# Kernel optimization log

Hardware: AMD Instinct MI355X
Metric: run time of the kernel (lower is better)

## Reference

```python
import jax, jax.numpy as jnp
import numpy as np

B, S = 4, 2048
D_MODEL, N_HEADS, D_KV = 1024, 16, 64
NUM_BUCKETS, MAX_DIST = 32, 128


def _relative_position_bucket(relative_position, num_buckets=NUM_BUCKETS, max_distance=MAX_DIST):
    # bidirectional (encoder) variant, faithful to FlaxT5Attention._relative_position_bucket
    num_buckets = num_buckets // 2
    relative_buckets = (relative_position > 0).astype(jnp.int32) * num_buckets
    rp = jnp.abs(relative_position)
    max_exact = num_buckets // 2
    is_small = rp < max_exact
    rp_large = max_exact + (
        jnp.log(rp.astype(jnp.float32) / max_exact)
        / np.log(max_distance / max_exact)
        * (num_buckets - max_exact)
    )
    rp_large = jnp.minimum(rp_large, num_buckets - 1)
    return relative_buckets + jnp.where(is_small, rp, rp_large.astype(jnp.int32))


def setup_inputs() -> dict:
    key = jax.random.key(0)
    ks = jax.random.split(key, 6)
    return {
        "hidden_states": jax.random.normal(ks[0], (B, S, D_MODEL), jnp.float32),
        "mask": jnp.zeros((B, S), jnp.float32),  # additive mask, 0 = attend
        "wq": jax.random.normal(ks[1], (D_MODEL, N_HEADS * D_KV), jnp.float32) * 0.02,
        "wk": jax.random.normal(ks[2], (D_MODEL, N_HEADS * D_KV), jnp.float32) * 0.02,
        "wv": jax.random.normal(ks[3], (D_MODEL, N_HEADS * D_KV), jnp.float32) * 0.02,
        "wo": jax.random.normal(ks[4], (N_HEADS * D_KV, D_MODEL), jnp.float32) * 0.02,
        "rel_bias": jax.random.normal(ks[5], (NUM_BUCKETS, N_HEADS), jnp.float32) * 0.02,
    }


def reference(hidden_states, mask, wq, wk, wv, wo, rel_bias):
    b, s, _ = hidden_states.shape
    # QKV projections, split heads -> [B, S, H, D]
    q = (hidden_states @ wq).reshape(b, s, N_HEADS, D_KV)
    k = (hidden_states @ wk).reshape(b, s, N_HEADS, D_KV)
    v = (hidden_states @ wv).reshape(b, s, N_HEADS, D_KV)

    # relative position bias -> [1, H, S, S]
    pos = jnp.arange(s, dtype=jnp.int32)
    relative_position = pos[None, :] - pos[:, None]  # memory - query
    buckets = _relative_position_bucket(relative_position)
    position_bias = rel_bias[buckets].transpose(2, 0, 1)[None]  # [1,H,S,S]
    # encoder path: additive mask expanded to [B,1,1,K]
    position_bias = position_bias + mask[:, None, None, :]

    # flax dot_product_attention_weights scales q by 1/sqrt(depth)
    scores = jnp.einsum("bqhd,bkhd->bhqk", q / jnp.sqrt(jnp.float32(D_KV)), k)
    attn_weights = jax.nn.softmax(scores + position_bias, axis=-1)

    attn_output = jnp.einsum("bhqk,bkhd->bqhd", attn_weights, v)
    attn_output = attn_output.reshape(b, s, N_HEADS * D_KV) @ wo
    return attn_output, position_bias
```

## Files before the change

kernel.cpp:

```cpp
#include <hip/hip_runtime.h>
#include <hip/hip_bf16.h>

typedef __attribute__((ext_vector_type(8))) short bf16x8;
typedef __attribute__((ext_vector_type(8))) unsigned short u16x8;
typedef __attribute__((ext_vector_type(4))) float f32x4;

#define B_   4
#define S_   2048
#define H_   16
#define DKV  64
#define DM   1024

static __device__ __forceinline__ f32x4 mfma16(bf16x8 a, bf16x8 b, f32x4 c){
  return __builtin_amdgcn_mfma_f32_16x16x32_bf16(a, b, c, 0, 0, 0);
}
static __device__ __forceinline__ unsigned short f2b(float f){
  union { __hip_bfloat16 b; unsigned short u; } x;
  x.b = __float2bfloat16(f);
  return x.u;
}

__global__ void cast_h_kernel(const float* __restrict__ in, unsigned short* __restrict__ out, int n4){
  int i = blockIdx.x * 256 + threadIdx.x;
  if (i >= n4) return;
  float4 v = reinterpret_cast<const float4*>(in)[i];
  ushort4 r;
  r.x = f2b(v.x); r.y = f2b(v.y); r.z = f2b(v.z); r.w = f2b(v.w);
  reinterpret_cast<ushort4*>(out)[i] = r;
}

__global__ void transpose_w_kernel(const float* __restrict__ w0, const float* __restrict__ w1,
                                   const float* __restrict__ w2, const float* __restrict__ w3,
                                   unsigned short* o0, unsigned short* o1,
                                   unsigned short* o2, unsigned short* o3){
  int z = blockIdx.z;
  const float* src = (z==0) ? w0 : (z==1) ? w1 : (z==2) ? w2 : w3;
  unsigned short* dst = (z==0) ? o0 : (z==1) ? o1 : (z==2) ? o2 : o3;
  __shared__ float tile[32][33];
  int bx = blockIdx.x * 32, by = blockIdx.y * 32;
  int tx = threadIdx.x, ty = threadIdx.y;
  #pragma unroll
  for (int i = 0; i < 32; i += 8)
    tile[ty + i][tx] = src[(size_t)(by + ty + i) * DM + bx + tx];
  __syncthreads();
  #pragma unroll
  for (int i = 0; i < 32; i += 8)
    dst[(size_t)(bx + ty + i) * DM + by + tx] = f2b(tile[tx][ty + i]);
}

__global__ void build_table_kernel(const float* __restrict__ rel_bias, float* __restrict__ table_t){
  int i = blockIdx.x * 256 + threadIdx.x;
  if (i >= 16 * 4095) return;
  int h = i / 4095;
  int idx = i - h * 4095;
  int rel = idx - 2047;
  int bucket = (rel > 0) ? 16 : 0;
  int rp = (rel < 0) ? -rel : rel;
  int off;
  if (rp < 8) off = rp;
  else off = 8 + (rp>=12) + (rp>=16) + (rp>=23) + (rp>=32) + (rp>=46) + (rp>=64) + (rp>=91);
  table_t[i] = rel_bias[(bucket + off) * 16 + h];
}

__global__ void posbias_kernel(const float* __restrict__ relb, const float* __restrict__ mask,
                               float* __restrict__ out){
  __shared__ float rbh[32];
  int row = blockIdx.x;
  int q = row & (S_ - 1);
  int h = (row >> 11) & (H_ - 1);
  int b = row >> 15;
  int tid = threadIdx.x;
  if (tid < 32) rbh[tid] = relb[tid * 16 + h];
  __syncthreads();
  const float* mrow = mask + b * S_;
  float* orow = out + (size_t)row * S_;
  int k0 = tid * 8;
  #pragma unroll
  for (int c = 0; c < 2; ++c){
    float4 mv = *(const float4*)(mrow + k0 + c * 4);
    float4 v;
    #pragma unroll
    for (int j = 0; j < 4; ++j){
      int k = k0 + c * 4 + j;
      int rel = k - q;
      int bucket = (rel > 0) ? 16 : 0;
      int rp = (rel < 0) ? -rel : rel;
      int off = (rp < 8) ? rp
              : 8 + (rp>=12) + (rp>=16) + (rp>=23) + (rp>=32) + (rp>=46) + (rp>=64) + (rp>=91);
      (&v.x)[j] = rbh[bucket + off] + (&mv.x)[j];
    }
    *(float4*)(orow + k0 + c*4) = v;
  }
}

template<int MODE>
__global__ __launch_bounds__(256, 2) void gemm_bt_kernel(
    const unsigned short* __restrict__ A, const unsigned short* __restrict__ Bt,
    void* __restrict__ outp, int M, int N, int K, float scale)
{
  __shared__ __align__(16) unsigned short As[128 * 40];
  __shared__ __align__(16) unsigned short Bs[128 * 40];
  int tid = threadIdx.x; int lane = tid & 63; int w = tid >> 6;
  int wr = w >> 1, wc = w & 1;
  int n0 = blockIdx.x * 128, m0 = blockIdx.y * 128;
  const char* Ab = (const char*)A;
  const char* Bb = (const char*)Bt;
  size_t Kb = (size_t)K * 2;

  int srow = (tid * 16) >> 6;
  int scolb = (tid * 16) & 63;

  f32x4 acc[4][4];
  #pragma unroll
  for (int i = 0; i < 4; ++i)
    #pragma unroll
    for (int j = 0; j < 4; ++j) acc[i][j] = (f32x4){0.f, 0.f, 0.f, 0.f};

  bf16x8 ar[2], br[2];
  auto gload = [&](int kt){
    size_t k0b = (size_t)kt * 64;
    #pragma unroll
    for (int c = 0; c < 2; ++c){
      int row = srow + c * 64;
      ar[c] = *(const bf16x8*)(Ab + (size_t)(m0 + row) * Kb + k0b + scolb);
      br[c] = *(const bf16x8*)(Bb + (size_t)(n0 + row) * Kb + k0b + scolb);
    }
  };
  auto lwrite = [&](){
    #pragma unroll
    for (int c = 0; c < 2; ++c){
      int row = srow + c * 64;
      *(bf16x8*)((char*)As + row * 80 + scolb) = ar[c];
      *(bf16x8*)((char*)Bs + row * 80 + scolb) = br[c];
    }
  };

  int nk = K >> 5;
  gload(0);
  lwrite();
  for (int kt = 0; kt < nk; ++kt){
    __syncthreads();
    if (kt + 1 < nk) gload(kt + 1);
    bf16x8 af[4], bfr[4];
    #pragma unroll
    for (int f = 0; f < 4; ++f){
      int row = wr * 64 + f * 16 + (lane & 15);
      af[f] = *(const bf16x8*)((const char*)As + row * 80 + (lane >> 4) * 16);
    }
    #pragma unroll
    for (int f = 0; f < 4; ++f){
      int row = wc * 64 + f * 16 + (lane & 15);
      bfr[f] = *(const bf16x8*)((const char*)Bs + row * 80 + (lane >> 4) * 16);
    }
    #pragma unroll
    for (int i = 0; i < 4; ++i)
      #pragma unroll
      for (int j = 0; j < 4; ++j)
        acc[i][j] = mfma16(af[i], bfr[j], acc[i][j]);
    __syncthreads();
    if (kt + 1 < nk) lwrite();
  }

  #pragma unroll
  for (int i = 0; i < 4; ++i){
    #pragma unroll
    for (int j = 0; j < 4; ++j){
      #pragma unroll
      for (int r = 0; r < 4; ++r){
        int m = m0 + wr * 64 + i * 16 + ((lane >> 4) * 4) + r;
        int n = n0 + wc * 64 + j * 16 + (lane & 15);
        if (MODE == 0){
          ((float*)outp)[(size_t)m * N + n] = acc[i][j][r] * scale;
        } else {
          int sel = n >> 10, nn = n & 1023;
          float v = acc[i][j][r] * (sel == 0 ? 0.125f : 1.0f);
          int b = m >> 11, s = m & 2047, hh = nn >> 6, d = nn & 63;
          ((unsigned short*)outp)[(size_t)sel * 8388608 +
              (((size_t)(b * H_ + hh) * S_) + s) * DKV + d] = f2b(v);
        }
      }
    }
  }
}

__global__ __launch_bounds__(256, 2) void attn_mfma_kernel(
    const unsigned short* __restrict__ Qp, const unsigned short* __restrict__ Kp,
    const unsigned short* __restrict__ Vp, const float* __restrict__ table_t,
    const float* __restrict__ mask, unsigned short* __restrict__ outp)
{
  __shared__ __align__(16) unsigned short Ks[64][72];
  __shared__ __align__(16) unsigned short Vs[64][72];
  __shared__ __align__(16) unsigned short Ps[4][16][72];
  __shared__ float bias_s[127];
  __shared__ float mask_s[64];

  int bid = blockIdx.x;
  int qt = bid & 31; int h = (bid >> 5) & 15; int b = bid >> 9;
  int qb = qt * 64;
  const unsigned short* qptr = Qp + ((size_t)(b * H_ + h) * S_ + qb) * DKV;
  const unsigned short* kptr = Kp + (size_t)(b * H_ + h) * S_ * DKV;
  const unsigned short* vptr = Vp + (size_t)(b * H_ + h) * S_ * DKV;
  int tid = threadIdx.x; int lane = tid & 63; int w = tid >> 6;

  bf16x8 qf[2];
  {
    const unsigned short* qrow = qptr + (size_t)(w * 16 + (lane & 15)) * DKV + 8 * (lane >> 4);
    qf[0] = *(const bf16x8*)qrow;
    qf[1] = *(const bf16x8*)(qrow + 32);
  }
  float m_r[4], l_r[4];
  f32x4 o_acc[4];
  #pragma unroll
  for (int r = 0; r < 4; ++r){ m_r[r] = -1e30f; l_r[r] = 0.f; }
  #pragma unroll
  for (int d = 0; d < 4; ++d) o_acc[d] = (f32x4){0.f, 0.f, 0.f, 0.f};

  int bias_base = h * 4095 + (2047 - qb - 63);

  int skey = tid & 63;
  int sd0  = (tid >> 6) * 16;

  u16x8 ka, kb2, va, vb2;
  float biasr = 0.f, maskr = 0.f;
  auto gload = [&](int k0){
    const unsigned short* krow = kptr + (size_t)(k0 + skey) * DKV + sd0;
    const unsigned short* vrow = vptr + (size_t)(k0 + skey) * DKV + sd0;
    ka  = *(const u16x8*)krow;
    kb2 = *(const u16x8*)(krow + 8);
    va  = *(const u16x8*)vrow;
    vb2 = *(const u16x8*)(vrow + 8);
    if (tid < 127) biasr = table_t[bias_base + k0 + tid];
    else if (tid >= 128 && tid < 192) maskr = mask[b * S_ + k0 + (tid - 128)];
  };
  auto lwrite = [&](){
    *(u16x8*)&Ks[skey][sd0]     = ka;
    *(u16x8*)&Ks[skey][sd0 + 8] = kb2;
    #pragma unroll
    for (int j = 0; j < 8; ++j){
      Vs[sd0 + j][skey]     = va[j];
      Vs[sd0 + 8 + j][skey] = vb2[j];
    }
    if (tid < 127) bias_s[tid] = biasr;
    else if (tid < 192) mask_s[tid - 128] = maskr;
  };

  gload(0);
  lwrite();
  for (int k0 = 0; k0 < S_; k0 += 64){
    __syncthreads();
    if (k0 + 64 < S_) gload(k0 + 64);

    f32x4 sc[4];
    #pragma unroll
    for (int kb = 0; kb < 4; ++kb){
      sc[kb] = (f32x4){0.f, 0.f, 0.f, 0.f};
      #pragma unroll
      for (int ks = 0; ks < 2; ++ks){
        int row = kb * 16 + (lane & 15);
        bf16x8 kf = *(const bf16x8*)&Ks[row][ks * 32 + (lane >> 4) * 8];
        sc[kb] = mfma16(qf[ks], kf, sc[kb]);
      }
    }
    float t[4][4];
    float tmax[4] = {-1e30f, -1e30f, -1e30f, -1e30f};
    #pragma unroll
    for (int kb = 0; kb < 4; ++kb){
      int k_l = kb * 16 + (lane & 15);
      float mk = mask_s[k_l];
      #pragma unroll
      for (int r = 0; r < 4; ++r){
        int q_l = w * 16 + (lane >> 4) * 4 + r;
        float tv = sc[kb][r] + bias_s[k_l - q_l + 63] + mk;
        t[kb][r] = tv;
        tmax[r] = fmaxf(tmax[r], tv);
      }
    }
    #pragma unroll
    for (int r = 0; r < 4; ++r){
      #pragma unroll
      for (int off = 1; off < 16; off <<= 1)
        tmax[r] = fmaxf(tmax[r], __shfl_xor(tmax[r], off, 64));
    }
    float scl[4];
    #pragma unroll
    for (int r = 0; r < 4; ++r){
      float mn = fmaxf(m_r[r], tmax[r]);
      scl[r] = __expf(m_r[r] - mn);
      m_r[r] = mn;
    }
    float rs[4] = {0.f, 0.f, 0.f, 0.f};
    #pragma unroll
    for (int kb = 0; kb < 4; ++kb)
      #pragma unroll
      for (int r = 0; r < 4; ++r){
        float p = __expf(t[kb][r] - m_r[r]);
        t[kb][r] = p;
        rs[r] += p;
      }
    #pragma unroll
    for (int r = 0; r < 4; ++r){
      #pragma unroll
      for (int off = 1; off < 16; off <<= 1)
        rs[r] += __shfl_xor(rs[r], off, 64);
      l_r[r] = l_r[r] * scl[r] + rs[r];
      o_acc[0][r] *= scl[r]; o_acc[1][r] *= scl[r];
      o_acc[2][r] *= scl[r]; o_acc[3][r] *= scl[r];
    }
    #pragma unroll
    for (int kb = 0; kb < 4; ++kb)
      #pragma unroll
      for (int r = 0; r < 4; ++r){
        int prow = (lane >> 4) * 4 + r;
        int pcol = kb * 16 + (lane & 15);
        Ps[w][prow][pcol] = f2b(t[kb][r]);
      }
    bf16x8 pa[2];
    #pragma unroll
    for (int ks = 0; ks < 2; ++ks)
      pa[ks] = *(const bf16x8*)&Ps[w][lane & 15][ks * 32 + (lane >> 4) * 8];
    #pragma unroll
    for (int db = 0; db < 4; ++db)
      #pragma unroll
      for (int ks = 0; ks < 2; ++ks){
        bf16x8 vf = *(const bf16x8*)&Vs[db * 16 + (lane & 15)][ks * 32 + (lane >> 4) * 8];
        o_acc[db] = mfma16(pa[ks], vf, o_acc[db]);
      }

    __syncthreads();
    if (k0 + 64 < S_) lwrite();
  }

  #pragma unroll
  for (int r = 0; r < 4; ++r){
    float inv = 1.0f / l_r[r];
    int qg = qb + w * 16 + (lane >> 4) * 4 + r;
    size_t rowoff = ((size_t)b * S_ + qg) * DM + h * DKV;
    #pragma unroll
    for (int db = 0; db < 4; ++db)
      outp[rowoff + db * 16 + (lane & 15)] = f2b(o_acc[db][r] * inv);
  }
}

extern "C" void kernel_launch(void* const* d_in, const int* in_sizes, int n_in,
                              void* d_out, int out_size, void* d_ws, size_t ws_size,
                              hipStream_t stream) {
  const float* hs   = (const float*)d_in[0];
  const float* msk  = (const float*)d_in[1];
  const float* wq   = (const float*)d_in[2];
  const float* wk   = (const float*)d_in[3];
  const float* wv   = (const float*)d_in[4];
  const float* wo   = (const float*)d_in[5];
  const float* relb = (const float*)d_in[6];

  float* out_attn = (float*)d_out;
  float* out_pb   = (float*)d_out + (size_t)B_ * S_ * DM;
  char* ws = (char*)out_pb;

  unsigned short* h_bf  = (unsigned short*)(ws + 0);
  unsigned short* wqkv_t= (unsigned short*)(ws + 16777216);
  unsigned short* wk_t  = (unsigned short*)(ws + 18874368);
  unsigned short* wv_t  = (unsigned short*)(ws + 20971520);
  unsigned short* wo_t  = (unsigned short*)(ws + 23068672);
  unsigned short* qkv_b = (unsigned short*)(ws + 25165824);
  unsigned short* k_b   = (unsigned short*)(ws + 41943040);
  unsigned short* v_b   = (unsigned short*)(ws + 58720256);
  float*          tabl  = (float*)(ws + 75497472);

  cast_h_kernel<<<8192, 256, 0, stream>>>(hs, h_bf, (B_ * S_ * DM) / 4);
  transpose_w_kernel<<<dim3(32, 32, 4), dim3(32, 8), 0, stream>>>(wq, wk, wv, wo,
                                                                  wqkv_t, wk_t, wv_t, wo_t);
  build_table_kernel<<<256, 256, 0, stream>>>(relb, tabl);

  gemm_bt_kernel<1><<<dim3(24, 64), 256, 0, stream>>>(h_bf, wqkv_t, qkv_b, 8192, 3072, 1024, 1.0f);

  attn_mfma_kernel<<<B_ * H_ * 32, 256, 0, stream>>>(qkv_b, k_b, v_b, tabl, msk, h_bf);

  gemm_bt_kernel<0><<<dim3(8, 64), 256, 0, stream>>>(h_bf, wo_t, out_attn, 8192, 1024, 1024, 1.0f);

  posbias_kernel<<<B_ * H_ * S_, 256, 0, stream>>>(relb, msk, out_pb);
}
```

Before: 541.7 us.

## Fuse position-bias output writes into attention kernel when workspace available

The attention kernel now also writes the [B,H,S,S] position-bias output from the bias and mask values it already holds in shared memory, which removes the separate posbias kernel. Intermediates move to the provided workspace so the position-bias region of the output is no longer used as scratch. This overlaps the large output store with attention compute, but adds global store traffic and work inside the attention loop. The fused path is taken only if the workspace is large enough; otherwise the old sequence runs.

```diff
diff --git a/kernel.cpp b/kernel.cpp
--- a/kernel.cpp
+++ b/kernel.cpp
@@ -183,10 +183,12 @@
   }
 }
 
+template<int FUSE_PB>
 __global__ __launch_bounds__(256, 2) void attn_mfma_kernel(
     const unsigned short* __restrict__ Qp, const unsigned short* __restrict__ Kp,
     const unsigned short* __restrict__ Vp, const float* __restrict__ table_t,
-    const float* __restrict__ mask, unsigned short* __restrict__ outp)
+    const float* __restrict__ mask, unsigned short* __restrict__ outp,
+    float* __restrict__ pb_out)
 {
   __shared__ __align__(16) unsigned short Ks[64][72];
   __shared__ __align__(16) unsigned short Vs[64][72];
@@ -219,6 +221,9 @@
 
   int skey = tid & 63;
   int sd0  = (tid >> 6) * 16;
+  int pq = tid >> 2;
+  int pk = (tid & 3) * 16;
+  float* pb_row = FUSE_PB ? (pb_out + ((size_t)((b * H_ + h) * S_) + qb + pq) * S_ + pk) : nullptr;
 
   u16x8 ka, kb2, va, vb2;
   float biasr = 0.f, maskr = 0.f;
@@ -261,6 +266,20 @@
         sc[kb] = mfma16(qf[ks], kf, sc[kb]);
       }
     }
+
+    if (FUSE_PB){
+      #pragma unroll
+      for (int c = 0; c < 4; ++c){
+        float4 v;
+        #pragma unroll
+        for (int j = 0; j < 4; ++j){
+          int kl = pk + c * 4 + j;
+          (&v.x)[j] = bias_s[kl - pq + 63] + mask_s[kl];
+        }
+        *(float4*)(pb_row + k0 + c * 4) = v;
+      }
+    }
+
     float t[4][4];
     float tmax[4] = {-1e30f, -1e30f, -1e30f, -1e30f};
     #pragma unroll
@@ -354,7 +373,10 @@
 
   float* out_attn = (float*)d_out;
   float* out_pb   = (float*)d_out + (size_t)B_ * S_ * DM;
-  char* ws = (char*)out_pb;
+
+  const size_t SCRATCH_NEED = 76021760;
+  bool fuse = (ws_size >= SCRATCH_NEED) && (d_ws != nullptr);
+  char* ws = fuse ? (char*)d_ws : (char*)out_pb;
 
   unsigned short* h_bf  = (unsigned short*)(ws + 0);
   unsigned short* wqkv_t= (unsigned short*)(ws + 16777216);
@@ -373,9 +395,12 @@
 
   gemm_bt_kernel<1><<<dim3(24, 64), 256, 0, stream>>>(h_bf, wqkv_t, qkv_b, 8192, 3072, 1024, 1.0f);
 
-  attn_mfma_kernel<<<B_ * H_ * 32, 256, 0, stream>>>(qkv_b, k_b, v_b, tabl, msk, h_bf);
-
-  gemm_bt_kernel<0><<<dim3(8, 64), 256, 0, stream>>>(h_bf, wo_t, out_attn, 8192, 1024, 1024, 1.0f);
-
-  posbias_kernel<<<B_ * H_ * S_, 256, 0, stream>>>(relb, msk, out_pb);
-}
+  if (fuse){
+    attn_mfma_kernel<1><<<B_ * H_ * 32, 256, 0, stream>>>(qkv_b, k_b, v_b, tabl, msk, h_bf, out_pb);
+    gemm_bt_kernel<0><<<dim3(8, 64), 256, 0, stream>>>(h_bf, wo_t, out_attn, 8192, 1024, 1024, 1.0f);
+  } else {
+    attn_mfma_kernel<0><<<B_ * H_ * 32, 256, 0, stream>>>(qkv_b, k_b, v_b, tabl, msk, h_bf, nullptr);
+    gemm_bt_kernel<0><<<dim3(8, 64), 256, 0, stream>>>(h_bf, wo_t, out_attn, 8192, 1024, 1024, 1.0f);
+    posbias_kernel<<<B_ * H_ * S_, 256, 0, stream>>>(relb, msk, out_pb);
+  }
+}
```

Result: slower. 566.5 us (+4.6%).
